# Optimization experiments

Measured on AMD Instinct MI355X. Metric: run time of the kernel, lower is better.

## Reference

```python
import jax, jax.numpy as jnp
import numpy as np
from jax import lax

BN_EPS = 1e-5
HEADS = 2


def dw_conv(x, w, stride, pad):
    # depthwise conv, NCHW, weight OIHW with I=1, groups=C
    return lax.conv_general_dilated(
        x, w, (stride, stride), [(pad, pad), (pad, pad)],
        dimension_numbers=('NCHW', 'OIHW', 'NCHW'),
        feature_group_count=x.shape[1])


def bn(x, g, b, m, v):
    inv = g * lax.rsqrt(v + BN_EPS)
    return (x - m[:, None, None]) * inv[:, None, None] + b[:, None, None]


def conv1x1(x, w, b):
    return jnp.einsum('bchw,oc->bohw', x, w) + b[:, None, None]


def setup_inputs() -> dict:
    key = jax.random.key(0)
    ks = jax.random.split(key, 20)
    B, C, H, W = 32, 128, 56, 56
    r = lambda i, shape, s=0.05: jax.random.normal(ks[i], shape, jnp.float32) * s
    return {
        'x': jax.random.normal(ks[0], (B, C, H, W), jnp.float32),
        'q_w': r(1, (C, C)), 'q_b': r(2, (C,)),
        'kv_w': r(3, (2 * C, C)), 'kv_b': r(4, (2 * C,)),
        'sr1_w': r(5, (C, 1, 4, 4), 0.2),
        'sr1_g': jax.random.uniform(ks[6], (C,), jnp.float32) + 0.5,
        'sr1_b': r(7, (C,)),
        'sr1_m': r(8, (C,)),
        'sr1_v': jax.random.uniform(ks[9], (C,), jnp.float32) + 0.5,
        'sr2_w': r(10, (C, 1, 1, 1), 0.5),
        'sr2_g': jax.random.uniform(ks[11], (C,), jnp.float32) + 0.5,
        'sr2_b': r(12, (C,)),
        'sr2_m': r(13, (C,)),
        'sr2_v': jax.random.uniform(ks[14], (C,), jnp.float32) + 0.5,
        'local_w': r(15, (C, 1, 3, 3), 0.2), 'local_b': r(16, (C,)),
    }


def reference(x, q_w, q_b, kv_w, kv_b,
              sr1_w, sr1_g, sr1_b, sr1_m, sr1_v,
              sr2_w, sr2_g, sr2_b, sr2_m, sr2_v,
              local_w, local_b):
    B, C, H, W = x.shape
    h = HEADS
    d = C // h
    scale = d ** -0.5

    # q projection: 1x1 conv -> [B, h, N, d]
    q = conv1x1(x, q_w, q_b)
    q = q.reshape(B, h, d, H * W).transpose(0, 1, 3, 2)

    # spatial reduction: depthwise strided conv + BN + ReLU, then depthwise 1x1 + BN
    kv = jax.nn.relu(bn(dw_conv(x, sr1_w, 4, 2), sr1_g, sr1_b, sr1_m, sr1_v))
    kv = bn(kv * sr2_w.reshape(C, 1, 1), sr2_g, sr2_b, sr2_m, sr2_v)

    # depthwise 3x3 local conv + residual
    kv = dw_conv(kv, local_w, 1, 1) + local_b[:, None, None] + kv

    # kv projection and split
    kvp = conv1x1(kv, kv_w, kv_b)
    k, v = jnp.split(kvp, 2, axis=1)
    Nk = k.shape[2] * k.shape[3]
    k = k.reshape(B, h, d, Nk)                       # [B,h,d,Nk]
    v = v.reshape(B, h, d, Nk).transpose(0, 1, 3, 2)  # [B,h,Nk,d]

    attn = jax.nn.softmax(jnp.einsum('bhnd,bhdm->bhnm', q, k) * scale, axis=-1)
    out = jnp.einsum('bhnm,bhmd->bhnd', attn, v)      # [B,h,N,d]
    return out.transpose(0, 1, 3, 2).reshape(B, C, H, W)
```

## Files before the change

kernel.cpp:

```cpp
#include <hip/hip_runtime.h>
#include <hip/hip_bf16.h>

#define B_    32
#define C_    128
#define H_    56
#define W_    56
#define N_    3136
#define HK_   15
#define NK_   225
#define D_    64

typedef __attribute__((ext_vector_type(8))) short bf16x8;
typedef __attribute__((ext_vector_type(4))) float f32x4;

__device__ __forceinline__ float b2f(unsigned short u) {
    union { float f; unsigned int i; } x;
    x.i = ((unsigned int)u) << 16;
    return x.f;
}
__device__ __forceinline__ unsigned short f2b(float f) {
    __hip_bfloat16 h = __float2bfloat16(f);
    return *(unsigned short*)&h;
}
__device__ __forceinline__ unsigned int pkbf(float a, float b) {
    return (unsigned int)f2b(a) | ((unsigned int)f2b(b) << 16);
}

__device__ __forceinline__ void gll16(const char* g, char* l) {
    __builtin_amdgcn_global_load_lds(
        (const __attribute__((address_space(1))) unsigned int*)g,
        (__attribute__((address_space(3))) unsigned int*)l,
        16, 0, 0);
}

__global__ __launch_bounds__(256) void prep_kernel(
        const float* __restrict__ x,
        const float* __restrict__ sr1_w, const float* __restrict__ sr1_g,
        const float* __restrict__ sr1_b, const float* __restrict__ sr1_m,
        const float* __restrict__ sr1_v, const float* __restrict__ sr2_w,
        const float* __restrict__ sr2_g, const float* __restrict__ sr2_b,
        const float* __restrict__ sr2_m, const float* __restrict__ sr2_v,
        const float* __restrict__ local_w, const float* __restrict__ local_b,
        const float* __restrict__ q_w, const float* __restrict__ q_b,
        const float* __restrict__ kv_w, const float* __restrict__ kv_b,
        float* __restrict__ kv2,
        unsigned short* __restrict__ wkq_sw, unsigned short* __restrict__ wv_sw,
        float* __restrict__ kwb, float* __restrict__ wb, float* __restrict__ qkb) {
    int tid = threadIdx.x;
    __shared__ union {
        struct { float xim[H_ * W_]; float kvt[HK_][HK_ + 1]; } sr;
        float wq[64][16];
    } U;

    if (blockIdx.x >= (unsigned)(B_ * C_)) {
        int bx = blockIdx.x - B_ * C_;
        int h  = bx >> 3, cg = bx & 7;
        for (int idx = tid; idx < 64 * 16; idx += 256)
            U.wq[idx >> 4][idx & 15] =
                q_w[(size_t)(h * 64 + (idx >> 4)) * 128 + cg * 16 + (idx & 15)];
        __syncthreads();
        {
            int cl = tid >> 4;
            int c  = cg * 16 + cl;
            int cp0 = (tid & 15) * 8;
            float acc[8];
#pragma unroll
            for (int i = 0; i < 8; ++i) acc[i] = 0.f;
            for (int e = 0; e < 64; ++e) {
                float wqv = U.wq[e][cl];
                const float* wkrow = kv_w + (size_t)(h * 64 + e) * 128 + cp0;
#pragma unroll
                for (int i = 0; i < 8; ++i) acc[i] += wqv * wkrow[i];
            }
            char* base = (char*)wkq_sw + (size_t)h * 32768 + (size_t)c * 256;
            ushort4 u0, u1;
            u0.x = f2b(acc[0] * 0.125f); u0.y = f2b(acc[1] * 0.125f);
            u0.z = f2b(acc[2] * 0.125f); u0.w = f2b(acc[3] * 0.125f);
            u1.x = f2b(acc[4] * 0.125f); u1.y = f2b(acc[5] * 0.125f);
            u1.z = f2b(acc[6] * 0.125f); u1.w = f2b(acc[7] * 0.125f);
            int sw = (c & 7) << 4;
            *(ushort4*)(base + ((cp0 * 2) ^ sw)) = u0;
            *(ushort4*)(base + ((cp0 * 2 + 8) ^ sw)) = u1;
        }
        if (tid < 16) {
            int cl = tid, c = cg * 16 + cl;
            float s = 0.f;
            for (int e = 0; e < 64; ++e) s += kv_b[h * 64 + e] * U.wq[e][cl];
            kwb[h * 128 + c] = s * 0.125f;
        }
        if (cg == 0) {
            if (tid < 128) {
                float s = 0.f;
                for (int e = 0; e < 64; ++e)
                    s += q_b[h * 64 + e] * kv_w[(size_t)(h * 64 + e) * 128 + tid];
                wb[h * 128 + tid] = s * 0.125f;
            }
            if (tid == 0) {
                float s = 0.f;
                for (int e = 0; e < 64; ++e) s += q_b[h * 64 + e] * kv_b[h * 64 + e];
                qkb[h] = s * 0.125f;
            }
        }
        if (cg == 1) {
            for (int idx = tid; idx < 64 * 128; idx += 256) {
                int e = idx >> 7, cp = idx & 127;
                unsigned short val = f2b(kv_w[(size_t)(128 + h * 64 + e) * 128 + cp]);
                *(unsigned short*)((char*)wv_sw + (size_t)h * 16384 + (size_t)e * 256 +
                                   (((cp * 2) ^ ((e & 7) << 4)))) = val;
            }
        }
        return;
    }

    int bc = blockIdx.x;
    int c  = bc & (C_ - 1);
    const float* xp = x + (size_t)bc * (H_ * W_);
    for (int idx = tid; idx < (H_ * W_) / 4; idx += 256)
        ((float4*)U.sr.xim)[idx] = ((const float4*)xp)[idx];
    __syncthreads();

    int p = tid;
    int oy = p / HK_, ox = p % HK_;
    if (p < NK_) {
        float s = 0.f;
#pragma unroll
        for (int ky = 0; ky < 4; ++ky) {
            int iy = oy * 4 - 2 + ky;
            if (iy < 0 || iy >= H_) continue;
#pragma unroll
            for (int kx = 0; kx < 4; ++kx) {
                int ix = ox * 4 - 2 + kx;
                if (ix < 0 || ix >= W_) continue;
                s += U.sr.xim[iy * W_ + ix] * sr1_w[c * 16 + ky * 4 + kx];
            }
        }
        float inv1 = sr1_g[c] * rsqrtf(sr1_v[c] + 1e-5f);
        s = (s - sr1_m[c]) * inv1 + sr1_b[c];
        s = fmaxf(s, 0.f);
        s *= sr2_w[c];
        float inv2 = sr2_g[c] * rsqrtf(sr2_v[c] + 1e-5f);
        s = (s - sr2_m[c]) * inv2 + sr2_b[c];
        U.sr.kvt[oy][ox] = s;
    }
    __syncthreads();
    if (p < NK_) {
        float v = U.sr.kvt[oy][ox] + local_b[c];
#pragma unroll
        for (int dy = -1; dy <= 1; ++dy) {
            int yy = oy + dy;
            if (yy < 0 || yy >= HK_) continue;
#pragma unroll
            for (int dx = -1; dx <= 1; ++dx) {
                int xx = ox + dx;
                if (xx < 0 || xx >= HK_) continue;
                v += U.sr.kvt[yy][xx] * local_w[c * 9 + (dy + 1) * 3 + (dx + 1)];
            }
        }
        kv2[(size_t)bc * NK_ + p] = v;
    }
}

#define L2B(r, cb) ((r) * 256 + ((cb) ^ (((r) & 7) << 4)))
__global__ __launch_bounds__(256, 2) void kvw_kernel(
        const float* __restrict__ kv2,
        const float* __restrict__ kv_b,
        const unsigned short* __restrict__ wkq_sw,
        const unsigned short* __restrict__ wv_sw,
        const float* __restrict__ kwb,
        const float* __restrict__ wb,
        const float* __restrict__ qkb,
        unsigned short* __restrict__ kw,
        float* __restrict__ bias_s,
        unsigned short* __restrict__ vbuf) {
    int b = blockIdx.x, h = blockIdx.y, mh = blockIdx.z;
    int bh = b * 2 + h;
    int m0 = mh * 64;
    int tid = threadIdx.x;
    int lo = tid & 15, hi = (tid >> 4) & 3, wid = tid >> 6;

    __shared__ char K2[16384];
    __shared__ char WQ[32768];
    __shared__ char WV[16384];

    {
        const char* srcQ = (const char*)wkq_sw + (size_t)h * 32768 + tid * 16;
        char* dstQ = WQ + wid * 1024;
#pragma unroll
        for (int i = 0; i < 8; ++i) gll16(srcQ + i * 4096, dstQ + i * 4096);
        const char* srcV = (const char*)wv_sw + (size_t)h * 16384 + tid * 16;
        char* dstV = WV + wid * 1024;
#pragma unroll
        for (int i = 0; i < 4; ++i) gll16(srcV + i * 4096, dstV + i * 4096);
    }
    {
        int j = tid & 63;
        int mg = m0 + j;
        bool val = (mg < NK_);
#pragma unroll
        for (int it = 0; it < 8; ++it) {
            int c0 = (tid >> 6) * 4 + it * 16;
            ushort4 u;
            if (val) {
                const float* kp = kv2 + ((size_t)b * 128 + c0) * NK_ + mg;
                u.x = f2b(kp[0]);
                u.y = f2b(kp[NK_]);
                u.z = f2b(kp[2 * NK_]);
                u.w = f2b(kp[3 * NK_]);
            } else { u.x = 0; u.y = 0; u.z = 0; u.w = 0; }
            *(ushort4*)(K2 + L2B(j, c0 * 2)) = u;
        }
    }
    __syncthreads();

    bf16x8 aq[4];
#pragma unroll
    for (int ks = 0; ks < 4; ++ks)
        aq[ks] = *(const bf16x8*)(K2 + L2B(wid * 16 + lo, ks * 64 + hi * 16));

    char* kwB = (char*)kw + (size_t)bh * 65536;
#pragma unroll
    for (int ct = 0; ct < 8; ++ct) {
        f32x4 acc = {0.f, 0.f, 0.f, 0.f};
#pragma unroll
        for (int ks = 0; ks < 4; ++ks) {
            bf16x8 bq = *(const bf16x8*)(WQ + L2B(ct * 16 + lo, ks * 64 + hi * 16));
            acc = __builtin_amdgcn_mfma_f32_16x16x32_bf16(aq[ks], bq, acc, 0, 0, 0);
        }
        int c = ct * 16 + lo;
        float kb = kwb[h * 128 + c];
#pragma unroll
        for (int r = 0; r < 4; ++r) {
            int mg = m0 + wid * 16 + hi * 4 + r;
            *(unsigned short*)(kwB + (size_t)mg * 256 + (((c * 2) ^ ((mg & 7) << 4)))) =
                f2b(acc[r] + kb);
        }
    }

    char* vB = (char*)vbuf + (size_t)bh * 32768;
#pragma unroll
    for (int et = 0; et < 4; ++et) {
        f32x4 acc = {0.f, 0.f, 0.f, 0.f};
#pragma unroll
        for (int ks = 0; ks < 4; ++ks) {
            bf16x8 bv = *(const bf16x8*)(WV + L2B(et * 16 + lo, ks * 64 + hi * 16));
            acc = __builtin_amdgcn_mfma_f32_16x16x32_bf16(aq[ks], bv, acc, 0, 0, 0);
        }
        int e = et * 16 + lo;
        float vb = kv_b[128 + h * 64 + e];
#pragma unroll
        for (int r = 0; r < 4; ++r) {
            int mg = m0 + wid * 16 + hi * 4 + r;
            *(unsigned short*)(vB + (size_t)e * 512 + (((mg * 2) ^ ((e & 7) << 4)))) =
                f2b(acc[r] + vb);
        }
    }

    if (tid < 64) {
        int mg = m0 + tid;
        float s;
        if (mg >= NK_) s = -1e30f;
        else {
            s = qkb[h];
            for (int i = 0; i < 128; ++i) {
                int cp = (i + (tid & 7) * 16) & 127;
                s += b2f(*(const unsigned short*)(K2 + L2B(tid, cp * 2))) * wb[h * 128 + cp];
            }
        }
        bias_s[(size_t)bh * 256 + mg] = s;
    }
}

#define XTB(j, c) ((j) * 256 + (((c) * 2) ^ (((j) & 15) << 4)))
#define KWB(rl, cb) ((rl) * 256 + ((cb) ^ (((rl) & 7) << 4)))
#define CVB(e, cb)  ((e) * 512 + ((cb) ^ (((e) & 7) << 4)))

__global__ __launch_bounds__(256, 3) void attn_kernel(
        const float* __restrict__ x,
        const unsigned short* __restrict__ kw,
        const float* __restrict__ bias_s,
        const unsigned short* __restrict__ vbuf,
        float* __restrict__ out) {
    int flat = blockIdx.x;
    int xcd  = flat & 7;
    int idx  = flat >> 3;
    int g    = idx / 49;
    int jt   = idx % 49;
    int bh   = g * 8 + xcd;
    int bb   = bh >> 1;
    int h    = bh & 1;
    int n0   = jt * 64;
    int tid = threadIdx.x;
    int lo  = tid & 15;
    int hi  = (tid >> 4) & 3;
    int wid = tid >> 6;
    int jw  = wid * 16;

    __shared__ char LA[16384];
    __shared__ char LC[32768];
    __shared__ float LBIAS[256];

    const char* kwG = (const char*)kw + (size_t)bh * 65536;
    const char* vG  = (const char*)vbuf + (size_t)bh * 32768;

    {
#pragma unroll
        for (int i = 0; i < 8; ++i)
            gll16(vG + i * 4096 + tid * 16, LC + i * 4096 + wid * 1024);
        if (wid == 0)
            gll16((const char*)(bias_s + (size_t)bh * 256) + tid * 16, (char*)LBIAS);
    }
#pragma unroll
    for (int it = 0; it < 8; ++it) {
        int j  = tid & 63;
        int c0 = (tid >> 6) * 4 + it * 16;
        const float* xp = x + ((size_t)bb * 128 + c0) * N_ + n0 + j;
        ushort4 u;
        u.x = f2b(xp[0]);
        u.y = f2b(xp[(size_t)N_]);
        u.z = f2b(xp[2 * (size_t)N_]);
        u.w = f2b(xp[3 * (size_t)N_]);
        *(ushort4*)(LA + XTB(j, c0)) = u;
    }
    asm volatile("s_waitcnt lgkmcnt(0)" ::: "memory");
    __builtin_amdgcn_s_barrier();

    bf16x8 aq[4];
#pragma unroll
    for (int ks = 0; ks < 4; ++ks)
        aq[ks] = *(const bf16x8*)(LA + XTB(jw + lo, ks * 32 + hi * 8));
    asm volatile("s_waitcnt lgkmcnt(0)" ::: "memory");
    __builtin_amdgcn_s_barrier();
    __builtin_amdgcn_sched_barrier(0);

    {
        const char* s0 = kwG + tid * 16;
        char* d0 = LA + wid * 1024;
        gll16(s0, d0); gll16(s0 + 4096, d0 + 4096);
        const char* s1 = kwG + 8192 + tid * 16;
        char* d1 = LA + 8192 + wid * 1024;
        gll16(s1, d1); gll16(s1 + 4096, d1 + 4096);
    }
    asm volatile("s_waitcnt vmcnt(2)" ::: "memory");
    __builtin_amdgcn_s_barrier();
    __builtin_amdgcn_sched_barrier(0);

    f32x4 s[15];
#pragma unroll
    for (int t = 0; t < 8; ++t) {
        char* Bt = LA + (t & 1) * 8192;
#pragma unroll
        for (int ml = 0; ml < 2; ++ml) {
            int mt = t * 2 + ml;
            if (mt >= 15) continue;
            f32x4 acc = {0.f, 0.f, 0.f, 0.f};
#pragma unroll
            for (int ks = 0; ks < 4; ++ks) {
                bf16x8 bk = *(const bf16x8*)(Bt + KWB(ml * 16 + lo, ks * 64 + hi * 16));
                acc = __builtin_amdgcn_mfma_f32_16x16x32_bf16(bk, aq[ks], acc, 0, 0, 0);
            }
            s[mt] = acc;
        }
        if (t < 6) {
            __builtin_amdgcn_s_barrier();
            const char* sn = kwG + (t + 2) * 8192 + tid * 16;
            char* dn = LA + (t & 1) * 8192 + wid * 1024;
            gll16(sn, dn); gll16(sn + 4096, dn + 4096);
        }
        if (t < 7) {
            if (t < 6) asm volatile("s_waitcnt vmcnt(2)" ::: "memory");
            else       asm volatile("s_waitcnt vmcnt(0)" ::: "memory");
            __builtin_amdgcn_s_barrier();
            __builtin_amdgcn_sched_barrier(0);
        }
    }

#pragma unroll
    for (int mt = 0; mt < 15; ++mt) {
        f32x4 bv = *(const f32x4*)&LBIAS[mt * 16 + hi * 4];
#pragma unroll
        for (int r = 0; r < 4; ++r) s[mt][r] += bv[r];
    }

    float mxv = s[0][0];
#pragma unroll
    for (int mt = 0; mt < 15; ++mt) {
#pragma unroll
        for (int r = 0; r < 4; ++r) mxv = fmaxf(mxv, s[mt][r]);
    }
    mxv = fmaxf(mxv, __shfl_xor(mxv, 16));
    mxv = fmaxf(mxv, __shfl_xor(mxv, 32));
    float smv = 0.f;
#pragma unroll
    for (int mt = 0; mt < 15; ++mt) {
#pragma unroll
        for (int r = 0; r < 4; ++r) {
            float pe = __expf(s[mt][r] - mxv);
            s[mt][r] = pe;
            smv += pe;
        }
    }
    smv += __shfl_xor(smv, 16);
    smv += __shfl_xor(smv, 32);
    float rinv = 1.f / smv;

    bf16x8 bp[8];
    int sA = lo + (hi & 1) * 32;
    int sB = sA + 16;
    bool lowm = (hi < 2);
#pragma unroll
    for (int ks = 0; ks < 8; ++ks) {
        int t0 = 2 * ks, t1 = 2 * ks + 1;
        unsigned int a0 = pkbf(s[t0][0], s[t0][1]);
        unsigned int a1 = pkbf(s[t0][2], s[t0][3]);
        unsigned int r0A = (unsigned int)__shfl((int)a0, sA);
        unsigned int r1A = (unsigned int)__shfl((int)a1, sA);
        unsigned int r0B = (unsigned int)__shfl((int)a0, sB);
        unsigned int r1B = (unsigned int)__shfl((int)a1, sB);
        unsigned int dw0, dw1, dw2, dw3;
        if (ks < 7) {
            unsigned int b0 = pkbf(s[t1][0], s[t1][1]);
            unsigned int b1 = pkbf(s[t1][2], s[t1][3]);
            unsigned int q0A = (unsigned int)__shfl((int)b0, sA);
            unsigned int q1A = (unsigned int)__shfl((int)b1, sA);
            unsigned int q0B = (unsigned int)__shfl((int)b0, sB);
            unsigned int q1B = (unsigned int)__shfl((int)b1, sB);
            dw0 = lowm ? r0A : q0A;
            dw1 = lowm ? r1A : q1A;
            dw2 = lowm ? r0B : q0B;
            dw3 = lowm ? r1B : q1B;
        } else {
            dw0 = lowm ? r0A : 0u;
            dw1 = lowm ? r1A : 0u;
            dw2 = lowm ? r0B : 0u;
            dw3 = lowm ? r1B : 0u;
        }
        uint4 d4 = {dw0, dw1, dw2, dw3};
        bp[ks] = *(bf16x8*)&d4;
    }

#pragma unroll
    for (int et = 0; et < 4; ++et) {
        f32x4 acc = {0.f, 0.f, 0.f, 0.f};
#pragma unroll
        for (int ks = 0; ks < 8; ++ks) {
            bf16x8 av = *(const bf16x8*)(LC + CVB(et * 16 + lo, ks * 64 + hi * 16));
            acc = __builtin_amdgcn_mfma_f32_16x16x32_bf16(av, bp[ks], acc, 0, 0, 0);
        }
        int e = et * 16 + hi * 4;
#pragma unroll
        for (int r = 0; r < 4; ++r)
            out[((size_t)bb * 128 + h * 64 + e + r) * N_ + n0 + jw + lo] = acc[r] * rinv;
    }
}

extern "C" void kernel_launch(void* const* d_in, const int* in_sizes, int n_in,
                              void* d_out, int out_size, void* d_ws, size_t ws_size,
                              hipStream_t stream) {
    const float* x       = (const float*)d_in[0];
    const float* q_w     = (const float*)d_in[1];
    const float* q_b     = (const float*)d_in[2];
    const float* kv_w    = (const float*)d_in[3];
    const float* kv_b    = (const float*)d_in[4];
    const float* sr1_w   = (const float*)d_in[5];
    const float* sr1_g   = (const float*)d_in[6];
    const float* sr1_b   = (const float*)d_in[7];
    const float* sr1_m   = (const float*)d_in[8];
    const float* sr1_v   = (const float*)d_in[9];
    const float* sr2_w   = (const float*)d_in[10];
    const float* sr2_g   = (const float*)d_in[11];
    const float* sr2_b   = (const float*)d_in[12];
    const float* sr2_m   = (const float*)d_in[13];
    const float* sr2_v   = (const float*)d_in[14];
    const float* local_w = (const float*)d_in[15];
    const float* local_b = (const float*)d_in[16];

    char* ws = (char*)d_ws;
    float* kv2              = (float*)(ws + 0);
    unsigned short* wkq_sw  = (unsigned short*)(ws + 3686400);
    unsigned short* wv_sw   = (unsigned short*)(ws + 3751936);
    unsigned short* kw      = (unsigned short*)(ws + 3784704);
    unsigned short* vbuf    = (unsigned short*)(ws + 7979008);
    float* bias_s           = (float*)(ws + 10076160);
    float* kwb              = (float*)(ws + 10141696);
    float* wb               = (float*)(ws + 10142720);
    float* qkb              = (float*)(ws + 10143744);

    prep_kernel<<<B_ * C_ + 16, 256, 0, stream>>>(
        x, sr1_w, sr1_g, sr1_b, sr1_m, sr1_v,
        sr2_w, sr2_g, sr2_b, sr2_m, sr2_v, local_w, local_b,
        q_w, q_b, kv_w, kv_b,
        kv2, wkq_sw, wv_sw, kwb, wb, qkb);
    kvw_kernel<<<dim3(B_, 2, 4), 256, 0, stream>>>(
        kv2, kv_b, wkq_sw, wv_sw, kwb, wb, qkb, kw, bias_s, vbuf);
    attn_kernel<<<3136, 256, 0, stream>>>(
        x, kw, bias_s, vbuf, (float*)d_out);
}
```

Baseline: 89.49 us.

## Load Q operand directly to registers, fold bias into MFMA init, use exp2 and packed bf16 converts

The attention kernel now loads each lane's x values straight from global memory into registers, which removes the LDS transpose round trip and two barriers. The K and V async loads are issued together so they overlap, and the vmcnt waits are adjusted to match. The bias is used as the MFMA accumulator's initial value instead of being added in a separate pass. The softmax scale is folded with log2(e) in the prep kernel so a raw v_exp_f32 can be used, and float-to-bf16 packing uses v_cvt_pk_bf16_f32. The register-direct x loads are strided per lane and less coalesced, and the tuned vmcnt counts must match the number of loads actually issued.

```diff
diff --git a/kernel.cpp b/kernel.cpp
--- a/kernel.cpp
+++ b/kernel.cpp
@@ -9,6 +9,7 @@
 #define HK_   15
 #define NK_   225
 #define D_    64
+#define SCL_  0.1803368801111731f
 
 typedef __attribute__((ext_vector_type(8))) short bf16x8;
 typedef __attribute__((ext_vector_type(4))) float f32x4;
@@ -22,8 +23,15 @@
     __hip_bfloat16 h = __float2bfloat16(f);
     return *(unsigned short*)&h;
 }
-__device__ __forceinline__ unsigned int pkbf(float a, float b) {
-    return (unsigned int)f2b(a) | ((unsigned int)f2b(b) << 16);
+__device__ __forceinline__ unsigned int cvtpk(float a, float b) {
+    unsigned int r;
+    asm("v_cvt_pk_bf16_f32 %0, %1, %2" : "=v"(r) : "v"(a), "v"(b));
+    return r;
+}
+__device__ __forceinline__ float exp2a(float x) {
+    float r;
+    asm("v_exp_f32 %0, %1" : "=v"(r) : "v"(x));
+    return r;
 }
 
 __device__ __forceinline__ void gll16(const char* g, char* l) {
@@ -74,10 +82,10 @@
             }
             char* base = (char*)wkq_sw + (size_t)h * 32768 + (size_t)c * 256;
             ushort4 u0, u1;
-            u0.x = f2b(acc[0] * 0.125f); u0.y = f2b(acc[1] * 0.125f);
-            u0.z = f2b(acc[2] * 0.125f); u0.w = f2b(acc[3] * 0.125f);
-            u1.x = f2b(acc[4] * 0.125f); u1.y = f2b(acc[5] * 0.125f);
-            u1.z = f2b(acc[6] * 0.125f); u1.w = f2b(acc[7] * 0.125f);
+            u0.x = f2b(acc[0] * SCL_); u0.y = f2b(acc[1] * SCL_);
+            u0.z = f2b(acc[2] * SCL_); u0.w = f2b(acc[3] * SCL_);
+            u1.x = f2b(acc[4] * SCL_); u1.y = f2b(acc[5] * SCL_);
+            u1.z = f2b(acc[6] * SCL_); u1.w = f2b(acc[7] * SCL_);
             int sw = (c & 7) << 4;
             *(ushort4*)(base + ((cp0 * 2) ^ sw)) = u0;
             *(ushort4*)(base + ((cp0 * 2 + 8) ^ sw)) = u1;
@@ -86,19 +94,19 @@
             int cl = tid, c = cg * 16 + cl;
             float s = 0.f;
             for (int e = 0; e < 64; ++e) s += kv_b[h * 64 + e] * U.wq[e][cl];
-            kwb[h * 128 + c] = s * 0.125f;
+            kwb[h * 128 + c] = s * SCL_;
         }
         if (cg == 0) {
             if (tid < 128) {
                 float s = 0.f;
                 for (int e = 0; e < 64; ++e)
                     s += q_b[h * 64 + e] * kv_w[(size_t)(h * 64 + e) * 128 + tid];
-                wb[h * 128 + tid] = s * 0.125f;
+                wb[h * 128 + tid] = s * SCL_;
             }
             if (tid == 0) {
                 float s = 0.f;
                 for (int e = 0; e < 64; ++e) s += q_b[h * 64 + e] * kv_b[h * 64 + e];
-                qkb[h] = s * 0.125f;
+                qkb[h] = s * SCL_;
             }
         }
         if (cg == 1) {
@@ -270,7 +278,6 @@
     }
 }
 
-#define XTB(j, c) ((j) * 256 + (((c) * 2) ^ (((j) & 15) << 4)))
 #define KWB(rl, cb) ((rl) * 256 + ((cb) ^ (((rl) & 7) << 4)))
 #define CVB(e, cb)  ((e) * 512 + ((cb) ^ (((e) & 7) << 4)))
 
@@ -302,45 +309,43 @@
     const char* kwG = (const char*)kw + (size_t)bh * 65536;
     const char* vG  = (const char*)vbuf + (size_t)bh * 32768;
 
+    const float* xb = x + ((size_t)bb * 128) * N_ + n0 + jw + lo;
+    float xf[4][8];
+#pragma unroll
+    for (int ks = 0; ks < 4; ++ks) {
+#pragma unroll
+        for (int i = 0; i < 8; ++i)
+            xf[ks][i] = xb[(size_t)(ks * 32 + hi * 8 + i) * N_];
+    }
+    __builtin_amdgcn_sched_barrier(0);
+
     {
-#pragma unroll
-        for (int i = 0; i < 8; ++i)
-            gll16(vG + i * 4096 + tid * 16, LC + i * 4096 + wid * 1024);
         if (wid == 0)
             gll16((const char*)(bias_s + (size_t)bh * 256) + tid * 16, (char*)LBIAS);
-    }
-#pragma unroll
-    for (int it = 0; it < 8; ++it) {
-        int j  = tid & 63;
-        int c0 = (tid >> 6) * 4 + it * 16;
-        const float* xp = x + ((size_t)bb * 128 + c0) * N_ + n0 + j;
-        ushort4 u;
-        u.x = f2b(xp[0]);
-        u.y = f2b(xp[(size_t)N_]);
-        u.z = f2b(xp[2 * (size_t)N_]);
-        u.w = f2b(xp[3 * (size_t)N_]);
-        *(ushort4*)(LA + XTB(j, c0)) = u;
-    }
-    asm volatile("s_waitcnt lgkmcnt(0)" ::: "memory");
-    __builtin_amdgcn_s_barrier();
-
-    bf16x8 aq[4];
-#pragma unroll
-    for (int ks = 0; ks < 4; ++ks)
-        aq[ks] = *(const bf16x8*)(LA + XTB(jw + lo, ks * 32 + hi * 8));
-    asm volatile("s_waitcnt lgkmcnt(0)" ::: "memory");
-    __builtin_amdgcn_s_barrier();
-    __builtin_amdgcn_sched_barrier(0);
-
-    {
         const char* s0 = kwG + tid * 16;
         char* d0 = LA + wid * 1024;
         gll16(s0, d0); gll16(s0 + 4096, d0 + 4096);
         const char* s1 = kwG + 8192 + tid * 16;
         char* d1 = LA + 8192 + wid * 1024;
         gll16(s1, d1); gll16(s1 + 4096, d1 + 4096);
-    }
-    asm volatile("s_waitcnt vmcnt(2)" ::: "memory");
+        const char* sc = vG + tid * 16;
+        char* dc = LC + wid * 1024;
+#pragma unroll
+        for (int i = 0; i < 8; ++i) gll16(sc + i * 4096, dc + i * 4096);
+    }
+
+    bf16x8 aq[4];
+#pragma unroll
+    for (int ks = 0; ks < 4; ++ks) {
+        uint4 u;
+        u.x = cvtpk(xf[ks][0], xf[ks][1]);
+        u.y = cvtpk(xf[ks][2], xf[ks][3]);
+        u.z = cvtpk(xf[ks][4], xf[ks][5]);
+        u.w = cvtpk(xf[ks][6], xf[ks][7]);
+        aq[ks] = *(bf16x8*)&u;
+    }
+
+    asm volatile("s_waitcnt vmcnt(10)" ::: "memory");
     __builtin_amdgcn_s_barrier();
     __builtin_amdgcn_sched_barrier(0);
 
@@ -352,7 +357,7 @@
         for (int ml = 0; ml < 2; ++ml) {
             int mt = t * 2 + ml;
             if (mt >= 15) continue;
-            f32x4 acc = {0.f, 0.f, 0.f, 0.f};
+            f32x4 acc = *(const f32x4*)&LBIAS[mt * 16 + hi * 4];
 #pragma unroll
             for (int ks = 0; ks < 4; ++ks) {
                 bf16x8 bk = *(const bf16x8*)(Bt + KWB(ml * 16 + lo, ks * 64 + hi * 16));
@@ -367,18 +372,12 @@
             gll16(sn, dn); gll16(sn + 4096, dn + 4096);
         }
         if (t < 7) {
-            if (t < 6) asm volatile("s_waitcnt vmcnt(2)" ::: "memory");
-            else       asm volatile("s_waitcnt vmcnt(0)" ::: "memory");
+            if (t == 0)      asm volatile("s_waitcnt vmcnt(10)" ::: "memory");
+            else if (t < 6)  asm volatile("s_waitcnt vmcnt(2)" ::: "memory");
+            else             asm volatile("s_waitcnt vmcnt(0)" ::: "memory");
             __builtin_amdgcn_s_barrier();
             __builtin_amdgcn_sched_barrier(0);
         }
-    }
-
-#pragma unroll
-    for (int mt = 0; mt < 15; ++mt) {
-        f32x4 bv = *(const f32x4*)&LBIAS[mt * 16 + hi * 4];
-#pragma unroll
-        for (int r = 0; r < 4; ++r) s[mt][r] += bv[r];
     }
 
     float mxv = s[0][0];
@@ -394,7 +393,7 @@
     for (int mt = 0; mt < 15; ++mt) {
 #pragma unroll
         for (int r = 0; r < 4; ++r) {
-            float pe = __expf(s[mt][r] - mxv);
+            float pe = exp2a(s[mt][r] - mxv);
             s[mt][r] = pe;
             smv += pe;
         }
@@ -410,16 +409,16 @@
 #pragma unroll
     for (int ks = 0; ks < 8; ++ks) {
         int t0 = 2 * ks, t1 = 2 * ks + 1;
-        unsigned int a0 = pkbf(s[t0][0], s[t0][1]);
-        unsigned int a1 = pkbf(s[t0][2], s[t0][3]);
+        unsigned int a0 = cvtpk(s[t0][0], s[t0][1]);
+        unsigned int a1 = cvtpk(s[t0][2], s[t0][3]);
         unsigned int r0A = (unsigned int)__shfl((int)a0, sA);
         unsigned int r1A = (unsigned int)__shfl((int)a1, sA);
         unsigned int r0B = (unsigned int)__shfl((int)a0, sB);
         unsigned int r1B = (unsigned int)__shfl((int)a1, sB);
         unsigned int dw0, dw1, dw2, dw3;
         if (ks < 7) {
-            unsigned int b0 = pkbf(s[t1][0], s[t1][1]);
-            unsigned int b1 = pkbf(s[t1][2], s[t1][3]);
+            unsigned int b0 = cvtpk(s[t1][0], s[t1][1]);
+            unsigned int b1 = cvtpk(s[t1][2], s[t1][3]);
             unsigned int q0A = (unsigned int)__shfl((int)b0, sA);
             unsigned int q1A = (unsigned int)__shfl((int)b1, sA);
             unsigned int q0B = (unsigned int)__shfl((int)b0, sB);
```

Measured after the change: 86.28 us. 1.04x faster.
